# Performance work log

Hardware: AMD Instinct MI355X
Metric: run time of the kernel (lower is better)

Reference implementation:

```python
import jax, jax.numpy as jnp
import numpy as np

NUM_CODES = 100000
DIM = 64
N = 65536   # B*T flattened visits
L = 48      # max codes per visit (padded with -1)
C = 1.0     # Poincare ball curvature
MIN_NORM = 1e-15
BALL_EPS = 1e-5   # geoopt projx boundary eps for float32
ATANH_EPS = 1e-7  # clamp artanh argument below 1


def _projx(x):
    # Poincare ball projection: pull points with norm >= (1-eps)/sqrt(c) back inside.
    sqrt_c = jnp.sqrt(C)
    norm = jnp.maximum(jnp.linalg.norm(x, axis=-1, keepdims=True), MIN_NORM)
    maxnorm = (1.0 - BALL_EPS) / sqrt_c
    return jnp.where(norm > maxnorm, x * (maxnorm / norm), x)


def setup_inputs() -> dict:
    key = jax.random.key(0)
    k1, k2, k3 = jax.random.split(key, 3)
    emb = jax.random.normal(k1, (NUM_CODES, DIM), dtype=jnp.float32) * 0.001
    emb = _projx(emb)
    ids = jax.random.randint(k2, (N, L), 0, NUM_CODES)
    pad = jax.random.uniform(k3, (N, L)) < 0.3
    code_ids = jnp.where(pad, jnp.int64(-1) if jax.config.jax_enable_x64 else -1, ids)
    return {"code_ids": code_ids, "emb": emb}


def reference(code_ids, emb):
    # code_ids: [N, L] int, -1 = padding; emb: [NUM_CODES, DIM] Poincare points.
    sqrt_c = jnp.sqrt(jnp.asarray(C, emb.dtype))
    mask = code_ids >= 0                               # [N, L]
    safe_ids = jnp.where(mask, code_ids, 0)
    x = emb[safe_ids]                                  # [N, L, D] gather
    # logmap0: artanh(sqrt(c)*||x||) * x / (sqrt(c)*||x||)
    norm = jnp.maximum(jnp.linalg.norm(x, axis=-1, keepdims=True), MIN_NORM)
    arg = jnp.minimum(sqrt_c * norm, 1.0 - ATANH_EPS)
    tangents = (jnp.arctanh(arg) / (sqrt_c * norm)) * x  # [N, L, D]
    m = mask[..., None].astype(emb.dtype)
    s = jnp.sum(tangents * m, axis=1)                  # [N, D]
    cnt = jnp.sum(m, axis=1)                           # [N, 1]
    return s / jnp.maximum(cnt, 1.0)                   # zeros for empty visits
```

## Files before the change

kernel.cpp:

```cpp
#include <hip/hip_runtime.h>


#define LCODES 48
#define DIM 64

typedef float vf4 __attribute__((ext_vector_type(4)));

__global__ __launch_bounds__(256)
void amax_kernel(const float* __restrict__ emb, unsigned* __restrict__ bmax,
                 long n4) {
    const uint4* __restrict__ u4 = reinterpret_cast<const uint4*>(emb);
    const long T = (long)gridDim.x * 256;
    unsigned m = 0;
    for (long i = (long)blockIdx.x * 256 + threadIdx.x; i < n4; i += 2 * T) {
        const uint4 a = u4[i];
        m = max(m, a.x & 0x7fffffffu);
        m = max(m, a.y & 0x7fffffffu);
        m = max(m, a.z & 0x7fffffffu);
        m = max(m, a.w & 0x7fffffffu);
        if (i + T < n4) {
            const uint4 b = u4[i + T];
            m = max(m, b.x & 0x7fffffffu);
            m = max(m, b.y & 0x7fffffffu);
            m = max(m, b.z & 0x7fffffffu);
            m = max(m, b.w & 0x7fffffffu);
        }
    }
    #pragma unroll
    for (int d = 1; d <= 32; d <<= 1)
        m = max(m, (unsigned)__shfl_xor((int)m, d, 64));
    __shared__ unsigned sm[4];
    if ((threadIdx.x & 63) == 0) sm[threadIdx.x >> 6] = m;
    __syncthreads();
    if (threadIdx.x == 0)
        bmax[blockIdx.x] = max(max(sm[0], sm[1]), max(sm[2], sm[3]));
}

__device__ __forceinline__ float global_amax1024(const unsigned* __restrict__ bmax) {
    const int lane = threadIdx.x & 63;
    unsigned m = 0;
    #pragma unroll
    for (int k = 0; k < 16; ++k)
        m = max(m, bmax[lane + 64 * k]);
    #pragma unroll
    for (int d = 1; d <= 32; d <<= 1)
        m = max(m, (unsigned)__shfl_xor((int)m, d, 64));
    return __uint_as_float(m);
}

__global__ __launch_bounds__(256)
void build_i8_kernel(const float* __restrict__ emb,
                     const unsigned* __restrict__ bmax,
                     unsigned char* __restrict__ tab,
                     float* __restrict__ qsout, int C) {
    const float amax = global_amax1024(bmax);
    const float qs   = amax * (1.0006f / 127.f);
    const float invq = (amax > 0.f) ? (127.f / (amax * 1.0006f)) : 0.f;
    if (blockIdx.x == 0 && threadIdx.x == 0) qsout[0] = qs;
    if (blockIdx.x == 0 && threadIdx.x < 16)
        reinterpret_cast<unsigned*>(tab + (size_t)C * DIM)[threadIdx.x] = 0u;

    const int tid  = threadIdx.x;
    const int lane = tid & 63;
    const int wave = tid >> 6;
    const int g = lane >> 3, s = lane & 7;
    const int r = blockIdx.x * 32 + wave * 8 + g;
    if (r >= C) return;

    const float4* __restrict__ emb4 = reinterpret_cast<const float4*>(emb);
    const float4 a = emb4[r * 16 + 2 * s];
    const float4 b = emb4[r * 16 + 2 * s + 1];

    float ss = a.x*a.x + a.y*a.y + a.z*a.z + a.w*a.w
             + b.x*b.x + b.y*b.y + b.z*b.z + b.w*b.w;
    ss += __shfl_xor(ss, 1, 64);
    ss += __shfl_xor(ss, 2, 64);
    ss += __shfl_xor(ss, 4, 64);

    float scale;
    if (__builtin_expect(ss > 0.04f, 0)) {
        const float norm = fmaxf(sqrtf(ss), 1e-15f);
        const float arg  = fminf(norm, 1.f - 1e-7f);
        scale = 0.5f * logf((1.f + arg) / (1.f - arg)) / norm;
    } else {
        scale = 1.f + ss * (0.33333333333f + ss * (0.2f + ss * 0.14285714285f));
    }
    scale *= invq;

    const float t[8] = { a.x*scale, a.y*scale, a.z*scale, a.w*scale,
                         b.x*scale, b.y*scale, b.z*scale, b.w*scale };
    unsigned u[8];
    #pragma unroll
    for (int k = 0; k < 8; ++k)
        u[k] = (unsigned)((int)rintf(t[k]) + 128);

    uint2 w;
    w.x = u[0] | (u[1] << 8) | (u[2] << 16) | (u[3] << 24);
    w.y = u[4] | (u[5] << 8) | (u[6] << 16) | (u[7] << 24);
    reinterpret_cast<uint2*>(tab)[r * 8 + s] = w;
}

__global__ __launch_bounds__(256)
void visit_gather_i8q2_kernel(const int* __restrict__ ids,
                              const unsigned char* __restrict__ tab,
                              const float* __restrict__ qsp,
                              float* __restrict__ out, int N, int C) {
    const float qs = qsp[0];

    const int tid  = threadIdx.x;
    const int lane = tid & 63;
    const int wave = tid >> 6;
    const int v0   = (blockIdx.x * 4 + wave) * 4;
    if (v0 >= N) return;

    __shared__ int sids[4][4 * LCODES];

    int m0 = -1, m1 = -1, m2 = -1, m3 = -1;
    if (lane < LCODES) {
        const long b = (long)v0 * LCODES;
        m0 = __builtin_nontemporal_load(&ids[b + lane]);
        if (v0 + 1 < N) m1 = __builtin_nontemporal_load(&ids[b + LCODES + lane]);
        if (v0 + 2 < N) m2 = __builtin_nontemporal_load(&ids[b + 2 * LCODES + lane]);
        if (v0 + 3 < N) m3 = __builtin_nontemporal_load(&ids[b + 3 * LCODES + lane]);
        sids[wave][lane]              = m0;
        sids[wave][LCODES + lane]     = m1;
        sids[wave][2 * LCODES + lane] = m2;
        sids[wave][3 * LCODES + lane] = m3;
    }
    const float cnt0 = (float)__popcll(__ballot(m0 >= 0));
    const float cnt1 = (float)__popcll(__ballot(m1 >= 0));
    const float cnt2 = (float)__popcll(__ballot(m2 >= 0));
    const float cnt3 = (float)__popcll(__ballot(m3 >= 0));

    const int v = lane >> 4;
    const int g = (lane >> 2) & 3;
    const int s = lane & 3;
    const uint4* __restrict__ tab4 = reinterpret_cast<const uint4*>(tab);
    const int* __restrict__ slid = &sids[wave][v * LCODES + g];

    unsigned aE[4] = {0,0,0,0}, aO[4] = {0,0,0,0};

    const int C2 = C >> 1;
    #pragma unroll
    for (int p = 0; p < 2; ++p) {
        const int lo = p ? C2 : 0;
        const int hi = p ? C  : C2;
        #pragma unroll
        for (int it = 0; it < LCODES / 4; ++it) {
            const int id = slid[4 * it];
            const bool inw = (id >= lo) & (id < hi);
            const unsigned base = ((unsigned)(inw ? id : C)) << 2;
            const uint4 w = tab4[base + s];
            aE[0] +=  w.x       & 0x00ff00ffu;
            aO[0] += (w.x >> 8) & 0x00ff00ffu;
            aE[1] +=  w.y       & 0x00ff00ffu;
            aO[1] += (w.y >> 8) & 0x00ff00ffu;
            aE[2] +=  w.z       & 0x00ff00ffu;
            aO[2] += (w.z >> 8) & 0x00ff00ffu;
            aE[3] +=  w.w       & 0x00ff00ffu;
            aO[3] += (w.w >> 8) & 0x00ff00ffu;
        }
        __builtin_amdgcn_sched_barrier(0);
    }

    #pragma unroll
    for (int d = 4; d <= 8; d <<= 1) {
        #pragma unroll
        for (int k = 0; k < 4; ++k) {
            aE[k] += (unsigned)__shfl_xor((int)aE[k], d, 64);
            aO[k] += (unsigned)__shfl_xor((int)aO[k], d, 64);
        }
    }

    const int f   = lane & 15;
    const int src = (lane & 0x30) | (f >> 2);
    const int kk  = lane & 3;
    unsigned e = 0, o = 0;
    #pragma unroll
    for (int k = 0; k < 4; ++k) {
        const unsigned ek = (unsigned)__shfl((int)aE[k], src, 64);
        const unsigned ok = (unsigned)__shfl((int)aO[k], src, 64);
        if (kk == k) { e = ek; o = ok; }
    }
    const float cnt = (v == 0) ? cnt0 : (v == 1) ? cnt1 : (v == 2) ? cnt2 : cnt3;
    const float qinv  = qs / fmaxf(cnt, 1.f);
    const float fbias = 128.f * cnt;
    vf4 r;
    r.x = ((float)(e  & 0xffffu) - fbias) * qinv;
    r.y = ((float)(o  & 0xffffu) - fbias) * qinv;
    r.z = ((float)(e  >> 16)     - fbias) * qinv;
    r.w = ((float)(o  >> 16)     - fbias) * qinv;
    if (v0 + v < N) {
        vf4* o4 = reinterpret_cast<vf4*>(out);
        __builtin_nontemporal_store(r, &o4[(long)v0 * 16 + lane]);
    }
}

__global__ __launch_bounds__(256, 4)
void visit_fp32_kernel(const int* __restrict__ ids,
                       const float* __restrict__ emb,
                       float* __restrict__ out, int N) {
    const int tid  = threadIdx.x;
    const int lane = tid & 63;
    const int wave = tid >> 6;
    const int v    = blockIdx.x * 4 + wave;
    if (v >= N) return;

    int myid = -1;
    if (lane < LCODES) myid = ids[(long)v * LCODES + lane];
    const unsigned long long valid = __ballot(myid >= 0);
    const float cnt = (float)__popcll(valid);
    const int g = lane >> 3, s = lane & 7;
    const float4* __restrict__ emb4 = reinterpret_cast<const float4*>(emb);
    float4 accA = make_float4(0.f,0.f,0.f,0.f), accB = make_float4(0.f,0.f,0.f,0.f);
    #pragma unroll
    for (int it = 0; it < LCODES / 8; ++it) {
        const int id = __shfl(myid, it * 8 + g, 64);
        const float keep = (id >= 0) ? 1.f : 0.f;
        const unsigned base = ((unsigned)(id >= 0 ? id : 0)) << 4;
        float4 a = emb4[base + s], b = emb4[base + 8 + s];
        float ss = a.x*a.x + a.y*a.y + a.z*a.z + a.w*a.w
                 + b.x*b.x + b.y*b.y + b.z*b.z + b.w*b.w;
        ss += __shfl_xor(ss, 1, 64);
        ss += __shfl_xor(ss, 2, 64);
        ss += __shfl_xor(ss, 4, 64);
        float scale;
        if (__builtin_expect(__any(ss > 0.04f), 0)) {
            const float norm = fmaxf(sqrtf(ss), 1e-15f);
            const float arg  = fminf(norm, 1.f - 1e-7f);
            scale = 0.5f * logf((1.f + arg) / (1.f - arg)) / norm;
        } else {
            scale = 1.f + ss * (0.33333333333f + ss * (0.2f + ss * 0.14285714285f));
        }
        scale *= keep;
        accA.x += a.x*scale; accA.y += a.y*scale; accA.z += a.z*scale; accA.w += a.w*scale;
        accB.x += b.x*scale; accB.y += b.y*scale; accB.z += b.z*scale; accB.w += b.w*scale;
    }
    #pragma unroll
    for (int d = 8; d <= 32; d <<= 1) {
        accA.x += __shfl_xor(accA.x, d, 64); accA.y += __shfl_xor(accA.y, d, 64);
        accA.z += __shfl_xor(accA.z, d, 64); accA.w += __shfl_xor(accA.w, d, 64);
        accB.x += __shfl_xor(accB.x, d, 64); accB.y += __shfl_xor(accB.y, d, 64);
        accB.z += __shfl_xor(accB.z, d, 64); accB.w += __shfl_xor(accB.w, d, 64);
    }
    if (lane < 8) {
        const float inv = 1.f / fmaxf(cnt, 1.f);
        float4* o = reinterpret_cast<float4*>(out) + (long)v * (DIM / 4);
        o[2*s]   = make_float4(accA.x*inv, accA.y*inv, accA.z*inv, accA.w*inv);
        o[2*s+1] = make_float4(accB.x*inv, accB.y*inv, accB.z*inv, accB.w*inv);
    }
}

extern "C" void kernel_launch(void* const* d_in, const int* in_sizes, int n_in,
                              void* d_out, int out_size, void* d_ws, size_t ws_size,
                              hipStream_t stream) {
    const int*   ids = (const int*)d_in[0];
    const float* emb = (const float*)d_in[1];
    float*       out = (float*)d_out;

    const int N = in_sizes[0] / LCODES;
    const int C = in_sizes[1] / DIM;

    const size_t tab_off = 8192;
    const size_t need = tab_off + (size_t)(C + 1) * DIM;

    if (ws_size >= need) {
        unsigned*      bmax = (unsigned*)d_ws;
        float*         qsp  = (float*)((char*)d_ws + 4096);
        unsigned char* tab  = (unsigned char*)d_ws + tab_off;

        const long n4 = (long)C * DIM / 4;
        hipLaunchKernelGGL(amax_kernel, dim3(1024), dim3(256), 0, stream,
                           emb, bmax, n4);
        const int blocksA = (C + 31) / 32;
        hipLaunchKernelGGL(build_i8_kernel, dim3(blocksA), dim3(256), 0, stream,
                           emb, bmax, tab, qsp, C);
        const int blocksB = (N + 15) / 16;
        hipLaunchKernelGGL(visit_gather_i8q2_kernel, dim3(blocksB), dim3(256), 0,
                           stream, ids, tab, qsp, out, N, C);
    } else {
        const int blocks = (N + 3) / 4;
        hipLaunchKernelGGL(visit_fp32_kernel, dim3(blocks), dim3(256), 0, stream,
                           ids, emb, out, N);
    }
}
```

Before: 106.9 us.

## Make gather kernel persistent with four visit groups per wave and block-synced passes

The int8 gather kernel now runs a fixed grid of 1024 blocks. Each wave processes four groups of four visits, loading all their ids and counts into shared memory up front. Both table-half passes loop over all groups, with a __syncthreads after each pass, which presumably keeps waves in step so each half of the table stays cache-resident. This puts more independent loads in flight per wave at the cost of more registers (launch bounds 4) and lower occupancy. The fast path is now limited to N up to 65536, and larger N falls back to the fp32 kernel.

```diff
diff --git a/kernel.cpp b/kernel.cpp
--- a/kernel.cpp
+++ b/kernel.cpp
@@ -3,6 +3,9 @@
 
 #define LCODES 48
 #define DIM 64
+#define K3_BLOCKS 1024
+#define CHUNKS (K3_BLOCKS * 4)
+#define NG 4
 
 typedef float vf4 __attribute__((ext_vector_type(4)));
 
@@ -100,45 +103,52 @@
     reinterpret_cast<uint2*>(tab)[r * 8 + s] = w;
 }
 
-__global__ __launch_bounds__(256)
-void visit_gather_i8q2_kernel(const int* __restrict__ ids,
-                              const unsigned char* __restrict__ tab,
-                              const float* __restrict__ qsp,
-                              float* __restrict__ out, int N, int C) {
+__global__ __launch_bounds__(256, 4)
+void visit_gather_i8p_kernel(const int* __restrict__ ids,
+                             const unsigned char* __restrict__ tab,
+                             const float* __restrict__ qsp,
+                             float* __restrict__ out, int N, int C) {
     const float qs = qsp[0];
 
-    const int tid  = threadIdx.x;
-    const int lane = tid & 63;
-    const int wave = tid >> 6;
-    const int v0   = (blockIdx.x * 4 + wave) * 4;
-    if (v0 >= N) return;
-
-    __shared__ int sids[4][4 * LCODES];
-
-    int m0 = -1, m1 = -1, m2 = -1, m3 = -1;
-    if (lane < LCODES) {
-        const long b = (long)v0 * LCODES;
-        m0 = __builtin_nontemporal_load(&ids[b + lane]);
-        if (v0 + 1 < N) m1 = __builtin_nontemporal_load(&ids[b + LCODES + lane]);
-        if (v0 + 2 < N) m2 = __builtin_nontemporal_load(&ids[b + 2 * LCODES + lane]);
-        if (v0 + 3 < N) m3 = __builtin_nontemporal_load(&ids[b + 3 * LCODES + lane]);
-        sids[wave][lane]              = m0;
-        sids[wave][LCODES + lane]     = m1;
-        sids[wave][2 * LCODES + lane] = m2;
-        sids[wave][3 * LCODES + lane] = m3;
-    }
-    const float cnt0 = (float)__popcll(__ballot(m0 >= 0));
-    const float cnt1 = (float)__popcll(__ballot(m1 >= 0));
-    const float cnt2 = (float)__popcll(__ballot(m2 >= 0));
-    const float cnt3 = (float)__popcll(__ballot(m3 >= 0));
+    const int tid   = threadIdx.x;
+    const int lane  = tid & 63;
+    const int wave  = tid >> 6;
+    const int chunk = blockIdx.x * 4 + wave;
+
+    __shared__ int   sids[4][NG][4 * 50];
+    __shared__ float scnt[4][NG][4];
+
+    #pragma unroll
+    for (int g = 0; g < NG; ++g) {
+        const int v0 = (g * CHUNKS + chunk) * 4;
+        int m0 = -1, m1 = -1, m2 = -1, m3 = -1;
+        if (lane < LCODES) {
+            const long b = (long)v0 * LCODES + lane;
+            if (v0     < N) m0 = __builtin_nontemporal_load(&ids[b]);
+            if (v0 + 1 < N) m1 = __builtin_nontemporal_load(&ids[b + LCODES]);
+            if (v0 + 2 < N) m2 = __builtin_nontemporal_load(&ids[b + 2 * LCODES]);
+            if (v0 + 3 < N) m3 = __builtin_nontemporal_load(&ids[b + 3 * LCODES]);
+            sids[wave][g][lane]           = m0;
+            sids[wave][g][50 + lane]      = m1;
+            sids[wave][g][100 + lane]     = m2;
+            sids[wave][g][150 + lane]     = m3;
+        }
+        const float c0 = (float)__popcll(__ballot(m0 >= 0));
+        const float c1 = (float)__popcll(__ballot(m1 >= 0));
+        const float c2 = (float)__popcll(__ballot(m2 >= 0));
+        const float c3 = (float)__popcll(__ballot(m3 >= 0));
+        if (lane == 0) {
+            scnt[wave][g][0] = c0;  scnt[wave][g][1] = c1;
+            scnt[wave][g][2] = c2;  scnt[wave][g][3] = c3;
+        }
+    }
 
     const int v = lane >> 4;
-    const int g = (lane >> 2) & 3;
+    const int gg = (lane >> 2) & 3;
     const int s = lane & 3;
     const uint4* __restrict__ tab4 = reinterpret_cast<const uint4*>(tab);
-    const int* __restrict__ slid = &sids[wave][v * LCODES + g];
-
-    unsigned aE[4] = {0,0,0,0}, aO[4] = {0,0,0,0};
+
+    unsigned aE[NG][4] = {{0}}, aO[NG][4] = {{0}};
 
     const int C2 = C >> 1;
     #pragma unroll
@@ -146,53 +156,61 @@
         const int lo = p ? C2 : 0;
         const int hi = p ? C  : C2;
         #pragma unroll
-        for (int it = 0; it < LCODES / 4; ++it) {
-            const int id = slid[4 * it];
-            const bool inw = (id >= lo) & (id < hi);
-            const unsigned base = ((unsigned)(inw ? id : C)) << 2;
-            const uint4 w = tab4[base + s];
-            aE[0] +=  w.x       & 0x00ff00ffu;
-            aO[0] += (w.x >> 8) & 0x00ff00ffu;
-            aE[1] +=  w.y       & 0x00ff00ffu;
-            aO[1] += (w.y >> 8) & 0x00ff00ffu;
-            aE[2] +=  w.z       & 0x00ff00ffu;
-            aO[2] += (w.z >> 8) & 0x00ff00ffu;
-            aE[3] +=  w.w       & 0x00ff00ffu;
-            aO[3] += (w.w >> 8) & 0x00ff00ffu;
+        for (int g = 0; g < NG; ++g) {
+            const int* __restrict__ slid = &sids[wave][g][v * 50 + gg];
+            #pragma unroll
+            for (int it = 0; it < LCODES / 4; ++it) {
+                const int id = slid[4 * it];
+                const bool inw = (id >= lo) & (id < hi);
+                const unsigned base = ((unsigned)(inw ? id : C)) << 2;
+                const uint4 w = tab4[base + s];
+                aE[g][0] +=  w.x       & 0x00ff00ffu;
+                aO[g][0] += (w.x >> 8) & 0x00ff00ffu;
+                aE[g][1] +=  w.y       & 0x00ff00ffu;
+                aO[g][1] += (w.y >> 8) & 0x00ff00ffu;
+                aE[g][2] +=  w.z       & 0x00ff00ffu;
+                aO[g][2] += (w.z >> 8) & 0x00ff00ffu;
+                aE[g][3] +=  w.w       & 0x00ff00ffu;
+                aO[g][3] += (w.w >> 8) & 0x00ff00ffu;
+            }
         }
         __builtin_amdgcn_sched_barrier(0);
-    }
-
-    #pragma unroll
-    for (int d = 4; d <= 8; d <<= 1) {
+        __syncthreads();
+    }
+
+    #pragma unroll
+    for (int g = 0; g < NG; ++g) {
+        #pragma unroll
+        for (int d = 4; d <= 8; d <<= 1) {
+            #pragma unroll
+            for (int k = 0; k < 4; ++k) {
+                aE[g][k] += (unsigned)__shfl_xor((int)aE[g][k], d, 64);
+                aO[g][k] += (unsigned)__shfl_xor((int)aO[g][k], d, 64);
+            }
+        }
+        const int f   = lane & 15;
+        const int src = (lane & 0x30) | (f >> 2);
+        const int kk  = lane & 3;
+        unsigned e = 0, o = 0;
         #pragma unroll
         for (int k = 0; k < 4; ++k) {
-            aE[k] += (unsigned)__shfl_xor((int)aE[k], d, 64);
-            aO[k] += (unsigned)__shfl_xor((int)aO[k], d, 64);
-        }
-    }
-
-    const int f   = lane & 15;
-    const int src = (lane & 0x30) | (f >> 2);
-    const int kk  = lane & 3;
-    unsigned e = 0, o = 0;
-    #pragma unroll
-    for (int k = 0; k < 4; ++k) {
-        const unsigned ek = (unsigned)__shfl((int)aE[k], src, 64);
-        const unsigned ok = (unsigned)__shfl((int)aO[k], src, 64);
-        if (kk == k) { e = ek; o = ok; }
-    }
-    const float cnt = (v == 0) ? cnt0 : (v == 1) ? cnt1 : (v == 2) ? cnt2 : cnt3;
-    const float qinv  = qs / fmaxf(cnt, 1.f);
-    const float fbias = 128.f * cnt;
-    vf4 r;
-    r.x = ((float)(e  & 0xffffu) - fbias) * qinv;
-    r.y = ((float)(o  & 0xffffu) - fbias) * qinv;
-    r.z = ((float)(e  >> 16)     - fbias) * qinv;
-    r.w = ((float)(o  >> 16)     - fbias) * qinv;
-    if (v0 + v < N) {
-        vf4* o4 = reinterpret_cast<vf4*>(out);
-        __builtin_nontemporal_store(r, &o4[(long)v0 * 16 + lane]);
+            const unsigned ek = (unsigned)__shfl((int)aE[g][k], src, 64);
+            const unsigned ok = (unsigned)__shfl((int)aO[g][k], src, 64);
+            if (kk == k) { e = ek; o = ok; }
+        }
+        const float cnt   = scnt[wave][g][v];
+        const float qinv  = qs / fmaxf(cnt, 1.f);
+        const float fbias = 128.f * cnt;
+        vf4 r;
+        r.x = ((float)(e & 0xffffu) - fbias) * qinv;
+        r.y = ((float)(o & 0xffffu) - fbias) * qinv;
+        r.z = ((float)(e >> 16)     - fbias) * qinv;
+        r.w = ((float)(o >> 16)     - fbias) * qinv;
+        const int v0 = (g * CHUNKS + chunk) * 4;
+        if (v0 + v < N) {
+            vf4* o4 = reinterpret_cast<vf4*>(out);
+            __builtin_nontemporal_store(r, &o4[(long)v0 * 16 + lane]);
+        }
     }
 }
 
@@ -264,7 +282,7 @@
     const size_t tab_off = 8192;
     const size_t need = tab_off + (size_t)(C + 1) * DIM;
 
-    if (ws_size >= need) {
+    if (ws_size >= need && N <= CHUNKS * NG * 4) {
         unsigned*      bmax = (unsigned*)d_ws;
         float*         qsp  = (float*)((char*)d_ws + 4096);
         unsigned char* tab  = (unsigned char*)d_ws + tab_off;
@@ -275,8 +293,7 @@
         const int blocksA = (C + 31) / 32;
         hipLaunchKernelGGL(build_i8_kernel, dim3(blocksA), dim3(256), 0, stream,
                            emb, bmax, tab, qsp, C);
-        const int blocksB = (N + 15) / 16;
-        hipLaunchKernelGGL(visit_gather_i8q2_kernel, dim3(blocksB), dim3(256), 0,
+        hipLaunchKernelGGL(visit_gather_i8p_kernel, dim3(K3_BLOCKS), dim3(256), 0,
                            stream, ids, tab, qsp, out, N, C);
     } else {
         const int blocks = (N + 3) / 4;
```

Result: slower. 203.7 us (+90.5%).
